# Optimization experiments

Hardware: AMD Instinct MI355X
Metric: run time of the kernel (lower is better)

Reference implementation:

```python
import jax, jax.numpy as jnp
import numpy as np

N_NODES = 50000
N_EDGES = 1600000
CHANNELS = 128
EXPANSION = 50
CUTOFF = 5.0
LOG2 = 0.6931471805599453


def shifted_softplus(x):
    return jax.nn.softplus(x) - LOG2


def gaussian_smearing(r, cutoff=CUTOFF, n=EXPANSION):
    # centers evenly spaced in [0, cutoff]; width set by spacing
    centers = jnp.linspace(0.0, cutoff, n, dtype=r.dtype)
    delta = centers[1] - centers[0]
    coef = 1.0 / (2.0 * delta * delta)
    d = r[:, None] - centers[None, :]          # [E, n]
    return jnp.exp(-coef * d * d)


def setup_inputs() -> dict:
    key = jax.random.key(0)
    ks = jax.random.split(key, 12)
    C, F = CHANNELS, EXPANSION

    def lin(k, fan_in, shape):
        bound = 1.0 / np.sqrt(fan_in)
        return jax.random.uniform(k, shape, jnp.float32, -bound, bound)

    return {
        "features": jax.random.normal(ks[0], (N_NODES, C), jnp.float32),
        "edge_distances": jax.random.uniform(ks[1], (N_EDGES,), jnp.float32) * CUTOFF,
        "W_lin": lin(ks[2], C, (C, C)),
        "Wf1": lin(ks[3], F, (F, C)), "bf1": lin(ks[4], F, (C,)),
        "Wf2": lin(ks[5], C, (C, C)), "bf2": lin(ks[6], C, (C,)),
        "Wm1": lin(ks[7], C, (C, C)), "bm1": lin(ks[8], C, (C,)),
        "Wm2": lin(ks[9], C, (C, C)), "bm2": lin(ks[10], C, (C,)),
        "senders": jax.random.randint(ks[11], (N_EDGES,), 0, N_NODES, jnp.int32),
        "receivers": jax.random.randint(jax.random.fold_in(key, 99), (N_EDGES,), 0, N_NODES, jnp.int32),
    }


def reference(features, edge_distances, W_lin, Wf1, bf1, Wf2, bf2,
              Wm1, bm1, Wm2, bm2, senders, receivers):
    # 1. linear transform of node features (no bias)
    h = features @ W_lin.T                                   # [N, C]
    # 2. learnable radial filter F(r_ij): Gaussian basis -> MLP
    basis = gaussian_smearing(edge_distances)                # [E, F]
    ef = shifted_softplus(basis @ Wf1 + bf1) @ Wf2 + bf2     # [E, C]
    # 3. gather neighbour features, elementwise multiply, scatter-sum
    messages = h[senders] * ef                               # [E, C]
    agg = jax.ops.segment_sum(messages, receivers, num_segments=N_NODES)  # [N, C]
    # 4. output MLP
    return shifted_softplus(agg @ Wm1 + bm1) @ Wm2 + bm2
```

## Files before the change

kernel.cpp:

```cpp
#include <hip/hip_runtime.h>
#include <hip/hip_bf16.h>
#include <math.h>

#define N_NODES 50000
#define N_EDGES 1600000
#define CH 128
#define NF 50
#define NR 8192
#define NB 2048
#define BUCKET_NODES 25
#define CAP 1024
#define PASSA_CHUNK 16384
#define NBLK_SCAT 98
#define NBLK_TB   128
#define NBLK_DH   782
#define NBLK_MLP  1563

constexpr float DELTA  = 5.0f / 49.0f;
constexpr float COEF   = 1.0f / (2.0f * DELTA * DELTA);
constexpr float LOG2_  = 0.6931471805599453f;
constexpr float RSCALE = (float)(NR - 1) / 5.0f;

typedef short  bf16x8 __attribute__((ext_vector_type(8)));
typedef float  f32x4  __attribute__((ext_vector_type(4)));
typedef unsigned short ushort_t;
typedef unsigned long long u64;

__device__ __forceinline__ float ssp(float x) {
    return fmaxf(x, 0.0f) + __logf(1.0f + __expf(-fabsf(x))) - LOG2_;
}
__device__ __forceinline__ ushort_t f2bf(float x) {
    __hip_bfloat16 b = __float2bfloat16(x);
    return *reinterpret_cast<ushort_t*>(&b);
}
__device__ __forceinline__ float bf2f(ushort_t u) {
    return __uint_as_float(((unsigned)u) << 16);
}
__device__ __forceinline__ float4 f4zero() { return make_float4(0.f, 0.f, 0.f, 0.f); }

__global__ __launch_bounds__(256) void k1_prep(const float* __restrict__ Wlin,
                                               const float* __restrict__ Wm1,
                                               const float* __restrict__ Wm2,
                                               const float* __restrict__ Wf1,
                                               const float* __restrict__ Wf2,
                                               ushort_t* __restrict__ wlhi,
                                               ushort_t* __restrict__ wllo,
                                               ushort_t* __restrict__ wm1hi,
                                               ushort_t* __restrict__ wm1lo,
                                               ushort_t* __restrict__ wm2hi,
                                               ushort_t* __restrict__ wm2lo,
                                               ushort_t* __restrict__ wf1t,
                                               ushort_t* __restrict__ wf2hi,
                                               ushort_t* __restrict__ wf2lo,
                                               int* __restrict__ bcnt) {
    const int tid = threadIdx.x;
    if (blockIdx.x == 64) {
        for (int i = tid; i < NB; i += 256) bcnt[i] = 0;
        return;
    }
    int idx = blockIdx.x * 256 + tid;
    int n = idx >> 7, k = idx & 127;
    {   float w = Wlin[(size_t)n * CH + k];
        ushort_t hi = f2bf(w); wlhi[n * CH + k] = hi; wllo[n * CH + k] = f2bf(w - bf2f(hi)); }
    {   float w = Wm1[(size_t)k * CH + n];
        ushort_t hi = f2bf(w); wm1hi[n * CH + k] = hi; wm1lo[n * CH + k] = f2bf(w - bf2f(hi)); }
    {   float w = Wm2[(size_t)k * CH + n];
        ushort_t hi = f2bf(w); wm2hi[n * CH + k] = hi; wm2lo[n * CH + k] = f2bf(w - bf2f(hi)); }
    if (k < 64) wf1t[n * 64 + k] = (k < NF) ? f2bf(Wf1[k * CH + n]) : (ushort_t)0;
    {   float w = Wf2[(size_t)k * CH + n];
        ushort_t hi = f2bf(w); wf2hi[n * CH + k] = hi; wf2lo[n * CH + k] = f2bf(w - bf2f(hi)); }
}

__device__ void scatter_body(char* smem, int blk,
                             const int* __restrict__ recv,
                             const int* __restrict__ send,
                             const float* __restrict__ dist,
                             int* __restrict__ bcnt,
                             u64* __restrict__ brec) {
    int* bcur   = (int*)smem;
    int* bbaseL = bcur + NB;
    const int tid = threadIdx.x;
    for (int i = tid; i < NB; i += 256) bcur[i] = 0;
    __syncthreads();
    const int e0 = blk * PASSA_CHUNK;
#pragma unroll 8
    for (int i = 0; i < 64; i++) {
        int e = e0 + tid + i * 256;
        if (e < N_EDGES) atomicAdd(&bcur[recv[e] / BUCKET_NODES], 1);
    }
    __syncthreads();
    for (int i = tid; i < NB; i += 256) {
        int c = bcur[i];
        bbaseL[i] = c ? atomicAdd(&bcnt[i], c) : 0;
        bcur[i] = 0;
    }
    __syncthreads();
#pragma unroll 4
    for (int i = 0; i < 64; i++) {
        int e = e0 + tid + i * 256;
        if (e < N_EDGES) {
            int r = recv[e];
            int b = r / BUCKET_NODES;
            int rank = bbaseL[b] + atomicAdd(&bcur[b], 1);
            if (rank < CAP) {
                float x = fminf(dist[e] * RSCALE, (float)(NR - 1));
                int ti = __float2int_rn(x);
                u64 rec = (u64)(unsigned)(send[e] | (r << 16)) | ((u64)ti << 32);
                brec[(size_t)b * CAP + rank] = rec;
            }
        }
    }
}

__device__ void table_body(char* smem, int blk,
                           const float* __restrict__ bf1,
                           const float* __restrict__ bf2,
                           const ushort_t* __restrict__ wf1t,
                           const ushort_t* __restrict__ wf2hi,
                           const ushort_t* __restrict__ wf2lo,
                           ushort_t* __restrict__ tabn) {
    ushort_t (*basis)[72] = (ushort_t (*)[72])smem;
    ushort_t (*t1s)[136]  = (ushort_t (*)[136])(smem + 64 * 72 * 2);
    const int tid = threadIdx.x;
    const int g0  = blk * 64;

    for (int i = tid; i < 64 * 64; i += 256) {
        int e = i >> 6, k = i & 63;
        float val = 0.f;
        if (k < NF) {
            float r = (float)(g0 + e) * (5.0f / (float)(NR - 1));
            float d = r - (float)k * DELTA;
            val = __expf(-COEF * d * d);
        }
        basis[e][k] = f2bf(val);
    }
    __syncthreads();

    const int lane = tid & 63;
    const int wv   = tid >> 6;
    const int row  = lane & 15;
    const int quad = lane >> 4;
    const int c0   = (2 * wv) * 16 + row;
    const int c1   = c0 + 16;

    f32x4 acc[2][4];
#pragma unroll
    for (int j = 0; j < 2; j++)
#pragma unroll
        for (int rt = 0; rt < 4; rt++) acc[j][rt] = (f32x4){0.f, 0.f, 0.f, 0.f};

#pragma unroll
    for (int kb = 0; kb < 64; kb += 32) {
        bf16x8 B0 = *(const bf16x8*)&wf1t[c0 * 64 + kb + quad * 8];
        bf16x8 B1 = *(const bf16x8*)&wf1t[c1 * 64 + kb + quad * 8];
#pragma unroll
        for (int rt = 0; rt < 4; rt++) {
            bf16x8 A = *(const bf16x8*)&basis[rt * 16 + row][kb + quad * 8];
            acc[0][rt] = __builtin_amdgcn_mfma_f32_16x16x32_bf16(A, B0, acc[0][rt], 0, 0, 0);
            acc[1][rt] = __builtin_amdgcn_mfma_f32_16x16x32_bf16(A, B1, acc[1][rt], 0, 0, 0);
        }
    }
    {
        float b1v[2] = { bf1[c0], bf1[c1] };
#pragma unroll
        for (int j = 0; j < 2; j++) {
            int c = j ? c1 : c0;
#pragma unroll
            for (int rt = 0; rt < 4; rt++)
#pragma unroll
                for (int rg = 0; rg < 4; rg++) {
                    int e = rt * 16 + quad * 4 + rg;
                    t1s[e][c] = f2bf(ssp(acc[j][rt][rg] + b1v[j]));
                }
        }
    }
    __syncthreads();

#pragma unroll
    for (int j = 0; j < 2; j++)
#pragma unroll
        for (int rt = 0; rt < 4; rt++) acc[j][rt] = (f32x4){0.f, 0.f, 0.f, 0.f};

#pragma unroll
    for (int kb = 0; kb < 128; kb += 32) {
        bf16x8 B0h = *(const bf16x8*)&wf2hi[c0 * CH + kb + quad * 8];
        bf16x8 B0l = *(const bf16x8*)&wf2lo[c0 * CH + kb + quad * 8];
        bf16x8 B1h = *(const bf16x8*)&wf2hi[c1 * CH + kb + quad * 8];
        bf16x8 B1l = *(const bf16x8*)&wf2lo[c1 * CH + kb + quad * 8];
#pragma unroll
        for (int rt = 0; rt < 4; rt++) {
            bf16x8 A = *(const bf16x8*)&t1s[rt * 16 + row][kb + quad * 8];
            acc[0][rt] = __builtin_amdgcn_mfma_f32_16x16x32_bf16(A, B0l, acc[0][rt], 0, 0, 0);
            acc[0][rt] = __builtin_amdgcn_mfma_f32_16x16x32_bf16(A, B0h, acc[0][rt], 0, 0, 0);
            acc[1][rt] = __builtin_amdgcn_mfma_f32_16x16x32_bf16(A, B1l, acc[1][rt], 0, 0, 0);
            acc[1][rt] = __builtin_amdgcn_mfma_f32_16x16x32_bf16(A, B1h, acc[1][rt], 0, 0, 0);
        }
    }
    {
        float b2v[2] = { bf2[c0], bf2[c1] };
#pragma unroll
        for (int j = 0; j < 2; j++) {
            int c = j ? c1 : c0;
#pragma unroll
            for (int rt = 0; rt < 4; rt++)
#pragma unroll
                for (int rg = 0; rg < 4; rg++) {
                    int g = g0 + rt * 16 + quad * 4 + rg;
                    tabn[(size_t)g * CH + c] = f2bf(acc[j][rt][rg] + b2v[j]);
                }
        }
    }
}

__device__ void dense_h_body(char* smem, int blk,
                             const float* __restrict__ X,
                             const ushort_t* __restrict__ Bhi,
                             const ushort_t* __restrict__ Blo,
                             ushort_t* __restrict__ Y) {
    ushort_t (*xs)[136] = (ushort_t (*)[136])smem;
    const int tid  = threadIdx.x;
    const int row0 = blk * 64;

#pragma unroll
    for (int i = 0; i < 8; i++) {
        int idx = tid + i * 256;
        int r   = idx >> 5;
        int c4  = (idx & 31) * 4;
        float4 v = (row0 + r < N_NODES) ? *(const float4*)&X[(size_t)(row0 + r) * CH + c4]
                                        : f4zero();
        ushort4 s;
        s.x = f2bf(v.x); s.y = f2bf(v.y); s.z = f2bf(v.z); s.w = f2bf(v.w);
        *(ushort4*)&xs[r][c4] = s;
    }
    __syncthreads();

    const int lane = tid & 63;
    const int wv   = tid >> 6;
    const int row  = lane & 15;
    const int quad = lane >> 4;
    const int c0   = (2 * wv) * 16 + row;
    const int c1   = c0 + 16;

    f32x4 acc[2][4];
#pragma unroll
    for (int j = 0; j < 2; j++)
#pragma unroll
        for (int rt = 0; rt < 4; rt++) acc[j][rt] = (f32x4){0.f, 0.f, 0.f, 0.f};

#pragma unroll
    for (int kb = 0; kb < 128; kb += 32) {
        bf16x8 B0h = *(const bf16x8*)&Bhi[(size_t)c0 * CH + kb + quad * 8];
        bf16x8 B0l = *(const bf16x8*)&Blo[(size_t)c0 * CH + kb + quad * 8];
        bf16x8 B1h = *(const bf16x8*)&Bhi[(size_t)c1 * CH + kb + quad * 8];
        bf16x8 B1l = *(const bf16x8*)&Blo[(size_t)c1 * CH + kb + quad * 8];
#pragma unroll
        for (int rt = 0; rt < 4; rt++) {
            bf16x8 A = *(const bf16x8*)&xs[rt * 16 + row][kb + quad * 8];
            acc[0][rt] = __builtin_amdgcn_mfma_f32_16x16x32_bf16(A, B0l, acc[0][rt], 0, 0, 0);
            acc[0][rt] = __builtin_amdgcn_mfma_f32_16x16x32_bf16(A, B0h, acc[0][rt], 0, 0, 0);
            acc[1][rt] = __builtin_amdgcn_mfma_f32_16x16x32_bf16(A, B1l, acc[1][rt], 0, 0, 0);
            acc[1][rt] = __builtin_amdgcn_mfma_f32_16x16x32_bf16(A, B1h, acc[1][rt], 0, 0, 0);
        }
    }

#pragma unroll
    for (int j = 0; j < 2; j++) {
        int c = j ? c1 : c0;
#pragma unroll
        for (int rt = 0; rt < 4; rt++)
#pragma unroll
            for (int rg = 0; rg < 4; rg++) {
                int r = row0 + rt * 16 + quad * 4 + rg;
                if (r < N_NODES) Y[(size_t)r * CH + c] = f2bf(acc[j][rt][rg]);
            }
    }
}

__global__ __launch_bounds__(256) void k2_mega(const int* __restrict__ recv,
                                               const int* __restrict__ send,
                                               const float* __restrict__ dist,
                                               int* __restrict__ bcnt,
                                               u64* __restrict__ brec,
                                               const float* __restrict__ bf1,
                                               const float* __restrict__ bf2,
                                               const ushort_t* __restrict__ wf1t,
                                               const ushort_t* __restrict__ wf2hi,
                                               const ushort_t* __restrict__ wf2lo,
                                               ushort_t* __restrict__ tabn,
                                               const float* __restrict__ X,
                                               const ushort_t* __restrict__ wlhi,
                                               const ushort_t* __restrict__ wllo,
                                               ushort_t* __restrict__ h) {
    __shared__ __align__(16) char smem[64 * 72 * 2 + 64 * 136 * 2];
    const int blk = blockIdx.x;
    if (blk < NBLK_SCAT) {
        scatter_body(smem, blk, recv, send, dist, bcnt, brec);
    } else if (blk < NBLK_SCAT + NBLK_TB) {
        table_body(smem, blk - NBLK_SCAT, bf1, bf2, wf1t, wf2hi, wf2lo, tabn);
    } else {
        dense_h_body(smem, blk - NBLK_SCAT - NBLK_TB, X, wlhi, wllo, h);
    }
}

__global__ __launch_bounds__(256) void sort_gather(const int* __restrict__ bcnt,
                                                   const u64* __restrict__ brec,
                                                   const ushort_t* __restrict__ h,
                                                   const ushort_t* __restrict__ tabn,
                                                   ushort_t* __restrict__ aggb) {
    __shared__ int shist[BUCKET_NODES];
    __shared__ int sbeg[BUCKET_NODES];
    __shared__ int sexc[BUCKET_NODES];
    __shared__ unsigned sout[CAP];
    const int b = blockIdx.x, tid = threadIdx.x;
    const int nbase = b * BUCKET_NODES;
    const int nn = min(BUCKET_NODES, N_NODES - nbase);
    if (nn <= 0) return;
    const int m = min(bcnt[b], CAP);
    const u64* my = brec + (size_t)b * CAP;

    for (int i = tid; i < nn; i += 256) shist[i] = 0;
    __syncthreads();
    for (int i = tid; i < m; i += 256) {
        u64 rec = __builtin_nontemporal_load(&my[i]);
        int l = (int)((rec >> 16) & 0xFFFF) - nbase;
        atomicAdd(&shist[l], 1);
    }
    __syncthreads();
    if (tid == 0) {
        int acc = 0;
#pragma unroll
        for (int l = 0; l < BUCKET_NODES; l++) {
            if (l < nn) { sexc[l] = acc; sbeg[l] = acc; acc += shist[l]; }
        }
    }
    __syncthreads();
    for (int i = tid; i < m; i += 256) {
        u64 rec = __builtin_nontemporal_load(&my[i]);
        int l = (int)((rec >> 16) & 0xFFFF) - nbase;
        int rank = atomicAdd(&sexc[l], 1);
        sout[rank] = (unsigned)(rec & 0xFFFF) | ((unsigned)((rec >> 32) & 0x3FFF) << 16);
    }
    __syncthreads();

    const int g  = tid >> 4;
    const int c8 = (tid & 15) * 8;
    for (int l = g; l < nn; l += 16) {
        const int beg = sbeg[l], end = sbeg[l] + shist[l];
        float acc[8];
#pragma unroll
        for (int j = 0; j < 8; j++) acc[j] = 0.f;

        int e = beg;
        for (; e + 8 <= end; e += 8) {
            unsigned v[8];
#pragma unroll
            for (int u = 0; u < 8; u++) v[u] = sout[e + u];
            bf16x8 hu[8], tn[8];
#pragma unroll
            for (int u = 0; u < 8; u++) {
                int s  = (int)(v[u] & 0xFFFF);
                int ti = (int)(v[u] >> 16);
                hu[u] = *(const bf16x8*)&h[(size_t)s * CH + c8];
                tn[u] = *(const bf16x8*)&tabn[(size_t)ti * CH + c8];
            }
#pragma unroll
            for (int u = 0; u < 8; u++)
#pragma unroll
                for (int j = 0; j < 8; j++)
                    acc[j] = fmaf(bf2f((ushort_t)hu[u][j]), bf2f((ushort_t)tn[u][j]), acc[j]);
        }
        for (; e + 4 <= end; e += 4) {
            unsigned v[4];
#pragma unroll
            for (int u = 0; u < 4; u++) v[u] = sout[e + u];
            bf16x8 hu[4], tn[4];
#pragma unroll
            for (int u = 0; u < 4; u++) {
                int s  = (int)(v[u] & 0xFFFF);
                int ti = (int)(v[u] >> 16);
                hu[u] = *(const bf16x8*)&h[(size_t)s * CH + c8];
                tn[u] = *(const bf16x8*)&tabn[(size_t)ti * CH + c8];
            }
#pragma unroll
            for (int u = 0; u < 4; u++)
#pragma unroll
                for (int j = 0; j < 8; j++)
                    acc[j] = fmaf(bf2f((ushort_t)hu[u][j]), bf2f((ushort_t)tn[u][j]), acc[j]);
        }
        for (; e < end; e++) {
            unsigned v = sout[e];
            int s  = (int)(v & 0xFFFF);
            int ti = (int)(v >> 16);
            bf16x8 hu = *(const bf16x8*)&h[(size_t)s * CH + c8];
            bf16x8 tn = *(const bf16x8*)&tabn[(size_t)ti * CH + c8];
#pragma unroll
            for (int j = 0; j < 8; j++)
                acc[j] = fmaf(bf2f((ushort_t)hu[j]), bf2f((ushort_t)tn[j]), acc[j]);
        }

        bf16x8 o;
#pragma unroll
        for (int j = 0; j < 8; j++) o[j] = (short)f2bf(acc[j]);
        __builtin_nontemporal_store(o, (bf16x8*)&aggb[(size_t)(nbase + l) * CH + c8]);
    }
}

__global__ __launch_bounds__(256) void out_mlp(const ushort_t* __restrict__ AGG,
                                               const ushort_t* __restrict__ B1hi,
                                               const ushort_t* __restrict__ B1lo,
                                               const float* __restrict__ bm1,
                                               const ushort_t* __restrict__ B2hi,
                                               const ushort_t* __restrict__ B2lo,
                                               const float* __restrict__ bm2,
                                               float* __restrict__ OUT, int M) {
    __shared__ ushort_t xs[32][136];
    const int tid  = threadIdx.x;
    const int row0 = blockIdx.x * 32;

#pragma unroll
    for (int i = 0; i < 2; i++) {
        int idx = tid + i * 256;
        int r   = idx >> 4;
        int c8  = (idx & 15) * 8;
        uint4 v = (row0 + r < M) ? *(const uint4*)&AGG[(size_t)(row0 + r) * CH + c8]
                                 : make_uint4(0, 0, 0, 0);
        *(uint4*)&xs[r][c8] = v;
    }
    __syncthreads();

    const int lane = tid & 63;
    const int wv   = tid >> 6;
    const int row  = lane & 15;
    const int quad = lane >> 4;
    const int c0   = (2 * wv) * 16 + row;
    const int c1   = c0 + 16;

    f32x4 acc[2][2];
#pragma unroll
    for (int j = 0; j < 2; j++)
#pragma unroll
        for (int rt = 0; rt < 2; rt++) acc[j][rt] = (f32x4){0.f, 0.f, 0.f, 0.f};

#pragma unroll
    for (int kb = 0; kb < 128; kb += 32) {
        bf16x8 B0h = *(const bf16x8*)&B1hi[(size_t)c0 * CH + kb + quad * 8];
        bf16x8 B0l = *(const bf16x8*)&B1lo[(size_t)c0 * CH + kb + quad * 8];
        bf16x8 B1h_ = *(const bf16x8*)&B1hi[(size_t)c1 * CH + kb + quad * 8];
        bf16x8 B1l_ = *(const bf16x8*)&B1lo[(size_t)c1 * CH + kb + quad * 8];
#pragma unroll
        for (int rt = 0; rt < 2; rt++) {
            bf16x8 A = *(const bf16x8*)&xs[rt * 16 + row][kb + quad * 8];
            acc[0][rt] = __builtin_amdgcn_mfma_f32_16x16x32_bf16(A, B0l, acc[0][rt], 0, 0, 0);
            acc[0][rt] = __builtin_amdgcn_mfma_f32_16x16x32_bf16(A, B0h, acc[0][rt], 0, 0, 0);
            acc[1][rt] = __builtin_amdgcn_mfma_f32_16x16x32_bf16(A, B1l_, acc[1][rt], 0, 0, 0);
            acc[1][rt] = __builtin_amdgcn_mfma_f32_16x16x32_bf16(A, B1h_, acc[1][rt], 0, 0, 0);
        }
    }
    __syncthreads();
    {
        float bv[2] = { bm1[c0], bm1[c1] };
#pragma unroll
        for (int j = 0; j < 2; j++) {
            int c = j ? c1 : c0;
#pragma unroll
            for (int rt = 0; rt < 2; rt++)
#pragma unroll
                for (int rg = 0; rg < 4; rg++)
                    xs[rt * 16 + quad * 4 + rg][c] = f2bf(ssp(acc[j][rt][rg] + bv[j]));
        }
    }
    __syncthreads();

#pragma unroll
    for (int j = 0; j < 2; j++)
#pragma unroll
        for (int rt = 0; rt < 2; rt++) acc[j][rt] = (f32x4){0.f, 0.f, 0.f, 0.f};

#pragma unroll
    for (int kb = 0; kb < 128; kb += 32) {
        bf16x8 B0h = *(const bf16x8*)&B2hi[(size_t)c0 * CH + kb + quad * 8];
        bf16x8 B0l = *(const bf16x8*)&B2lo[(size_t)c0 * CH + kb + quad * 8];
        bf16x8 B1h_ = *(const bf16x8*)&B2hi[(size_t)c1 * CH + kb + quad * 8];
        bf16x8 B1l_ = *(const bf16x8*)&B2lo[(size_t)c1 * CH + kb + quad * 8];
#pragma unroll
        for (int rt = 0; rt < 2; rt++) {
            bf16x8 A = *(const bf16x8*)&xs[rt * 16 + row][kb + quad * 8];
            acc[0][rt] = __builtin_amdgcn_mfma_f32_16x16x32_bf16(A, B0l, acc[0][rt], 0, 0, 0);
            acc[0][rt] = __builtin_amdgcn_mfma_f32_16x16x32_bf16(A, B0h, acc[0][rt], 0, 0, 0);
            acc[1][rt] = __builtin_amdgcn_mfma_f32_16x16x32_bf16(A, B1l_, acc[1][rt], 0, 0, 0);
            acc[1][rt] = __builtin_amdgcn_mfma_f32_16x16x32_bf16(A, B1h_, acc[1][rt], 0, 0, 0);
        }
    }
    {
        float bv[2] = { bm2[c0], bm2[c1] };
#pragma unroll
        for (int j = 0; j < 2; j++) {
            int c = j ? c1 : c0;
#pragma unroll
            for (int rt = 0; rt < 2; rt++)
#pragma unroll
                for (int rg = 0; rg < 4; rg++) {
                    int r = row0 + rt * 16 + quad * 4 + rg;
                    if (r < M) OUT[(size_t)r * CH + c] = acc[j][rt][rg] + bv[j];
                }
        }
    }
}

extern "C" void kernel_launch(void* const* d_in, const int* in_sizes, int n_in,
                              void* d_out, int out_size, void* d_ws, size_t ws_size,
                              hipStream_t stream) {
    const float* features = (const float*)d_in[0];
    const float* dist     = (const float*)d_in[1];
    const float* W_lin    = (const float*)d_in[2];
    const float* Wf1      = (const float*)d_in[3];
    const float* bf1      = (const float*)d_in[4];
    const float* Wf2      = (const float*)d_in[5];
    const float* bf2      = (const float*)d_in[6];
    const float* Wm1      = (const float*)d_in[7];
    const float* bm1      = (const float*)d_in[8];
    const float* Wm2      = (const float*)d_in[9];
    const float* bm2      = (const float*)d_in[10];
    const int* senders    = (const int*)d_in[11];
    const int* receivers  = (const int*)d_in[12];
    float* out = (float*)d_out;

    u64* brec       = (u64*)d_ws;
    ushort_t* h     = (ushort_t*)(brec + (size_t)NB * CAP);
    ushort_t* aggb  = h + (size_t)N_NODES * CH;
    ushort_t* tabn  = aggb + (size_t)N_NODES * CH;
    int* bcnt       = (int*)(tabn + (size_t)NR * CH);
    ushort_t* wlhi  = (ushort_t*)(bcnt + NB);
    ushort_t* wllo  = wlhi  + CH * CH;
    ushort_t* wm1hi = wllo  + CH * CH;
    ushort_t* wm1lo = wm1hi + CH * CH;
    ushort_t* wm2hi = wm1lo + CH * CH;
    ushort_t* wm2lo = wm2hi + CH * CH;
    ushort_t* wf1t  = wm2lo + CH * CH;
    ushort_t* wf2hi = wf1t  + CH * 64;
    ushort_t* wf2lo = wf2hi + CH * CH;

    k1_prep<<<65, 256, 0, stream>>>(W_lin, Wm1, Wm2, Wf1, Wf2,
                                    wlhi, wllo, wm1hi, wm1lo, wm2hi, wm2lo,
                                    wf1t, wf2hi, wf2lo, bcnt);

    k2_mega<<<NBLK_SCAT + NBLK_TB + NBLK_DH, 256, 0, stream>>>(
        receivers, senders, dist, bcnt, brec,
        bf1, bf2, wf1t, wf2hi, wf2lo, tabn,
        features, wlhi, wllo, h);

    sort_gather<<<NB, 256, 0, stream>>>(bcnt, brec, h, tabn, aggb);

    out_mlp<<<NBLK_MLP, 256, 0, stream>>>(aggb, wm1hi, wm1lo, bm1,
                                          wm2hi, wm2lo, bm2, out, N_NODES);
}
```

Before: 298.1 us.

## Fuse output MLP into sort-gather kernel and shrink scatter chunk size

Folds the output MLP into the per-bucket gather kernel. Each block keeps its aggregated rows (25 nodes, padded to 32) in shared memory and runs both MFMA layers on them directly, so the bf16 agg buffer no longer makes a round trip through global memory and one launch goes away. It also cuts the scatter chunk per block from 16384 to 4096 edges to get more scatter blocks, and writes bucket records with nontemporal stores. The cost is that the MLP now runs on 32-row tiles with only 25 valid rows, which wastes some MFMA work, and the gather kernel uses more LDS, which may lower occupancy.

Result: faster. 270.1 us (-9.4%).

```diff
diff --git a/kernel.cpp b/kernel.cpp
--- a/kernel.cpp
+++ b/kernel.cpp
@@ -10,11 +10,10 @@
 #define NB 2048
 #define BUCKET_NODES 25
 #define CAP 1024
-#define PASSA_CHUNK 16384
-#define NBLK_SCAT 98
+#define PASSA_CHUNK 4096
+#define NBLK_SCAT 391
 #define NBLK_TB   128
 #define NBLK_DH   782
-#define NBLK_MLP  1563
 
 constexpr float DELTA  = 5.0f / 49.0f;
 constexpr float COEF   = 1.0f / (2.0f * DELTA * DELTA);
@@ -83,8 +82,8 @@
     for (int i = tid; i < NB; i += 256) bcur[i] = 0;
     __syncthreads();
     const int e0 = blk * PASSA_CHUNK;
-#pragma unroll 8
-    for (int i = 0; i < 64; i++) {
+#pragma unroll
+    for (int i = 0; i < 16; i++) {
         int e = e0 + tid + i * 256;
         if (e < N_EDGES) atomicAdd(&bcur[recv[e] / BUCKET_NODES], 1);
     }
@@ -95,8 +94,8 @@
         bcur[i] = 0;
     }
     __syncthreads();
-#pragma unroll 4
-    for (int i = 0; i < 64; i++) {
+#pragma unroll
+    for (int i = 0; i < 16; i++) {
         int e = e0 + tid + i * 256;
         if (e < N_EDGES) {
             int r = recv[e];
@@ -106,7 +105,7 @@
                 float x = fminf(dist[e] * RSCALE, (float)(NR - 1));
                 int ti = __float2int_rn(x);
                 u64 rec = (u64)(unsigned)(send[e] | (r << 16)) | ((u64)ti << 32);
-                brec[(size_t)b * CAP + rank] = rec;
+                __builtin_nontemporal_store(rec, &brec[(size_t)b * CAP + rank]);
             }
         }
     }
@@ -302,15 +301,22 @@
     }
 }
 
-__global__ __launch_bounds__(256) void sort_gather(const int* __restrict__ bcnt,
-                                                   const u64* __restrict__ brec,
-                                                   const ushort_t* __restrict__ h,
-                                                   const ushort_t* __restrict__ tabn,
-                                                   ushort_t* __restrict__ aggb) {
+__global__ __launch_bounds__(256) void sort_gather_mlp(const int* __restrict__ bcnt,
+                                                       const u64* __restrict__ brec,
+                                                       const ushort_t* __restrict__ h,
+                                                       const ushort_t* __restrict__ tabn,
+                                                       const ushort_t* __restrict__ B1hi,
+                                                       const ushort_t* __restrict__ B1lo,
+                                                       const float* __restrict__ bm1,
+                                                       const ushort_t* __restrict__ B2hi,
+                                                       const ushort_t* __restrict__ B2lo,
+                                                       const float* __restrict__ bm2,
+                                                       float* __restrict__ OUT) {
     __shared__ int shist[BUCKET_NODES];
     __shared__ int sbeg[BUCKET_NODES];
     __shared__ int sexc[BUCKET_NODES];
     __shared__ unsigned sout[CAP];
+    __shared__ __align__(16) ushort_t at[32][136];
     const int b = blockIdx.x, tid = threadIdx.x;
     const int nbase = b * BUCKET_NODES;
     const int nn = min(BUCKET_NODES, N_NODES - nbase);
@@ -319,6 +325,10 @@
     const u64* my = brec + (size_t)b * CAP;
 
     for (int i = tid; i < nn; i += 256) shist[i] = 0;
+    for (int i = tid; i < 32 * 17; i += 256) {
+        bf16x8 z = (bf16x8){0, 0, 0, 0, 0, 0, 0, 0};
+        *(bf16x8*)&at[i / 17][(i % 17) * 8] = z;
+    }
     __syncthreads();
     for (int i = tid; i < m; i += 256) {
         u64 rec = __builtin_nontemporal_load(&my[i]);
@@ -342,89 +352,68 @@
     }
     __syncthreads();
 
-    const int g  = tid >> 4;
-    const int c8 = (tid & 15) * 8;
-    for (int l = g; l < nn; l += 16) {
-        const int beg = sbeg[l], end = sbeg[l] + shist[l];
-        float acc[8];
-#pragma unroll
-        for (int j = 0; j < 8; j++) acc[j] = 0.f;
-
-        int e = beg;
-        for (; e + 8 <= end; e += 8) {
-            unsigned v[8];
-#pragma unroll
-            for (int u = 0; u < 8; u++) v[u] = sout[e + u];
-            bf16x8 hu[8], tn[8];
-#pragma unroll
-            for (int u = 0; u < 8; u++) {
-                int s  = (int)(v[u] & 0xFFFF);
-                int ti = (int)(v[u] >> 16);
-                hu[u] = *(const bf16x8*)&h[(size_t)s * CH + c8];
-                tn[u] = *(const bf16x8*)&tabn[(size_t)ti * CH + c8];
+    {
+        const int g  = tid >> 4;
+        const int c8 = (tid & 15) * 8;
+        for (int l = g; l < nn; l += 16) {
+            const int beg = sbeg[l], end = sbeg[l] + shist[l];
+            float acc[8];
+#pragma unroll
+            for (int j = 0; j < 8; j++) acc[j] = 0.f;
+
+            int e = beg;
+            for (; e + 8 <= end; e += 8) {
+                unsigned v[8];
+#pragma unroll
+                for (int u = 0; u < 8; u++) v[u] = sout[e + u];
+                bf16x8 hu[8], tn[8];
+#pragma unroll
+                for (int u = 0; u < 8; u++) {
+                    int s  = (int)(v[u] & 0xFFFF);
+                    int ti = (int)(v[u] >> 16);
+                    hu[u] = *(const bf16x8*)&h[(size_t)s * CH + c8];
+                    tn[u] = *(const bf16x8*)&tabn[(size_t)ti * CH + c8];
+                }
+#pragma unroll
+                for (int u = 0; u < 8; u++)
+#pragma unroll
+                    for (int j = 0; j < 8; j++)
+                        acc[j] = fmaf(bf2f((ushort_t)hu[u][j]), bf2f((ushort_t)tn[u][j]), acc[j]);
             }
-#pragma unroll
-            for (int u = 0; u < 8; u++)
+            for (; e + 4 <= end; e += 4) {
+                unsigned v[4];
+#pragma unroll
+                for (int u = 0; u < 4; u++) v[u] = sout[e + u];
+                bf16x8 hu[4], tn[4];
+#pragma unroll
+                for (int u = 0; u < 4; u++) {
+                    int s  = (int)(v[u] & 0xFFFF);
+                    int ti = (int)(v[u] >> 16);
+                    hu[u] = *(const bf16x8*)&h[(size_t)s * CH + c8];
+                    tn[u] = *(const bf16x8*)&tabn[(size_t)ti * CH + c8];
+                }
+#pragma unroll
+                for (int u = 0; u < 4; u++)
+#pragma unroll
+                    for (int j = 0; j < 8; j++)
+                        acc[j] = fmaf(bf2f((ushort_t)hu[u][j]), bf2f((ushort_t)tn[u][j]), acc[j]);
+            }
+            for (; e < end; e++) {
+                unsigned v = sout[e];
+                int s  = (int)(v & 0xFFFF);
+                int ti = (int)(v >> 16);
+                bf16x8 hu = *(const bf16x8*)&h[(size_t)s * CH + c8];
+                bf16x8 tn = *(const bf16x8*)&tabn[(size_t)ti * CH + c8];
 #pragma unroll
                 for (int j = 0; j < 8; j++)
-                    acc[j] = fmaf(bf2f((ushort_t)hu[u][j]), bf2f((ushort_t)tn[u][j]), acc[j]);
-        }
-        for (; e + 4 <= end; e += 4) {
-            unsigned v[4];
-#pragma unroll
-            for (int u = 0; u < 4; u++) v[u] = sout[e + u];
-            bf16x8 hu[4], tn[4];
-#pragma unroll
-            for (int u = 0; u < 4; u++) {
-                int s  = (int)(v[u] & 0xFFFF);
-                int ti = (int)(v[u] >> 16);
-                hu[u] = *(const bf16x8*)&h[(size_t)s * CH + c8];
-                tn[u] = *(const bf16x8*)&tabn[(size_t)ti * CH + c8];
+                    acc[j] = fmaf(bf2f((ushort_t)hu[j]), bf2f((ushort_t)tn[j]), acc[j]);
             }
-#pragma unroll
-            for (int u = 0; u < 4; u++)
-#pragma unroll
-                for (int j = 0; j < 8; j++)
-                    acc[j] = fmaf(bf2f((ushort_t)hu[u][j]), bf2f((ushort_t)tn[u][j]), acc[j]);
-        }
-        for (; e < end; e++) {
-            unsigned v = sout[e];
-            int s  = (int)(v & 0xFFFF);
-            int ti = (int)(v >> 16);
-            bf16x8 hu = *(const bf16x8*)&h[(size_t)s * CH + c8];
-            bf16x8 tn = *(const bf16x8*)&tabn[(size_t)ti * CH + c8];
-#pragma unroll
-            for (int j = 0; j < 8; j++)
-                acc[j] = fmaf(bf2f((ushort_t)hu[j]), bf2f((ushort_t)tn[j]), acc[j]);
-        }
-
-        bf16x8 o;
-#pragma unroll
-        for (int j = 0; j < 8; j++) o[j] = (short)f2bf(acc[j]);
-        __builtin_nontemporal_store(o, (bf16x8*)&aggb[(size_t)(nbase + l) * CH + c8]);
-    }
-}
-
-__global__ __launch_bounds__(256) void out_mlp(const ushort_t* __restrict__ AGG,
-                                               const ushort_t* __restrict__ B1hi,
-                                               const ushort_t* __restrict__ B1lo,
-                                               const float* __restrict__ bm1,
-                                               const ushort_t* __restrict__ B2hi,
-                                               const ushort_t* __restrict__ B2lo,
-                                               const float* __restrict__ bm2,
-                                               float* __restrict__ OUT, int M) {
-    __shared__ ushort_t xs[32][136];
-    const int tid  = threadIdx.x;
-    const int row0 = blockIdx.x * 32;
-
-#pragma unroll
-    for (int i = 0; i < 2; i++) {
-        int idx = tid + i * 256;
-        int r   = idx >> 4;
-        int c8  = (idx & 15) * 8;
-        uint4 v = (row0 + r < M) ? *(const uint4*)&AGG[(size_t)(row0 + r) * CH + c8]
-                                 : make_uint4(0, 0, 0, 0);
-        *(uint4*)&xs[r][c8] = v;
+
+            bf16x8 o;
+#pragma unroll
+            for (int j = 0; j < 8; j++) o[j] = (short)f2bf(acc[j]);
+            *(bf16x8*)&at[l][c8] = o;
+        }
     }
     __syncthreads();
 
@@ -449,7 +438,7 @@
         bf16x8 B1l_ = *(const bf16x8*)&B1lo[(size_t)c1 * CH + kb + quad * 8];
 #pragma unroll
         for (int rt = 0; rt < 2; rt++) {
-            bf16x8 A = *(const bf16x8*)&xs[rt * 16 + row][kb + quad * 8];
+            bf16x8 A = *(const bf16x8*)&at[rt * 16 + row][kb + quad * 8];
             acc[0][rt] = __builtin_amdgcn_mfma_f32_16x16x32_bf16(A, B0l, acc[0][rt], 0, 0, 0);
             acc[0][rt] = __builtin_amdgcn_mfma_f32_16x16x32_bf16(A, B0h, acc[0][rt], 0, 0, 0);
             acc[1][rt] = __builtin_amdgcn_mfma_f32_16x16x32_bf16(A, B1l_, acc[1][rt], 0, 0, 0);
@@ -466,7 +455,7 @@
             for (int rt = 0; rt < 2; rt++)
 #pragma unroll
                 for (int rg = 0; rg < 4; rg++)
-                    xs[rt * 16 + quad * 4 + rg][c] = f2bf(ssp(acc[j][rt][rg] + bv[j]));
+                    at[rt * 16 + quad * 4 + rg][c] = f2bf(ssp(acc[j][rt][rg] + bv[j]));
         }
     }
     __syncthreads();
@@ -484,7 +473,7 @@
         bf16x8 B1l_ = *(const bf16x8*)&B2lo[(size_t)c1 * CH + kb + quad * 8];
 #pragma unroll
         for (int rt = 0; rt < 2; rt++) {
-            bf16x8 A = *(const bf16x8*)&xs[rt * 16 + row][kb + quad * 8];
+            bf16x8 A = *(const bf16x8*)&at[rt * 16 + row][kb + quad * 8];
             acc[0][rt] = __builtin_amdgcn_mfma_f32_16x16x32_bf16(A, B0l, acc[0][rt], 0, 0, 0);
             acc[0][rt] = __builtin_amdgcn_mfma_f32_16x16x32_bf16(A, B0h, acc[0][rt], 0, 0, 0);
             acc[1][rt] = __builtin_amdgcn_mfma_f32_16x16x32_bf16(A, B1l_, acc[1][rt], 0, 0, 0);
@@ -500,8 +489,8 @@
             for (int rt = 0; rt < 2; rt++)
 #pragma unroll
                 for (int rg = 0; rg < 4; rg++) {
-                    int r = row0 + rt * 16 + quad * 4 + rg;
-                    if (r < M) OUT[(size_t)r * CH + c] = acc[j][rt][rg] + bv[j];
+                    int r = rt * 16 + quad * 4 + rg;
+                    if (r < nn) OUT[(size_t)(nbase + r) * CH + c] = acc[j][rt][rg] + bv[j];
                 }
         }
     }
@@ -527,8 +516,7 @@
 
     u64* brec       = (u64*)d_ws;
     ushort_t* h     = (ushort_t*)(brec + (size_t)NB * CAP);
-    ushort_t* aggb  = h + (size_t)N_NODES * CH;
-    ushort_t* tabn  = aggb + (size_t)N_NODES * CH;
+    ushort_t* tabn  = h + (size_t)N_NODES * CH;
     int* bcnt       = (int*)(tabn + (size_t)NR * CH);
     ushort_t* wlhi  = (ushort_t*)(bcnt + NB);
     ushort_t* wllo  = wlhi  + CH * CH;
@@ -549,8 +537,7 @@
         bf1, bf2, wf1t, wf2hi, wf2lo, tabn,
         features, wlhi, wllo, h);
 
-    sort_gather<<<NB, 256, 0, stream>>>(bcnt, brec, h, tabn, aggb);
-
-    out_mlp<<<NBLK_MLP, 256, 0, stream>>>(aggb, wm1hi, wm1lo, bm1,
-                                          wm2hi, wm2lo, bm2, out, N_NODES);
-}
+    sort_gather_mlp<<<NB, 256, 0, stream>>>(bcnt, brec, h, tabn,
+                                            wm1hi, wm1lo, bm1,
+                                            wm2hi, wm2lo, bm2, out);
+}
```
